# Performance work log

Hardware: AMD Instinct MI355X
Metric: run time of the kernel (lower is better)

Reference implementation:

```python
import jax, jax.numpy as jnp
import numpy as np

SEQ, NSTEPS = 8192, 2048
IDIM, HDIM, NL = 256, 1024, 4


def setup_inputs() -> dict:
    key = jax.random.key(0)
    ks = jax.random.split(key, 6)
    s = 0.02  # small init so tanh recurrence stays well-conditioned
    return {
        "xs": jax.random.normal(ks[0], (SEQ, IDIM), dtype=jnp.float32),
        "Wx0": jax.random.normal(ks[1], (IDIM, HDIM), dtype=jnp.float32) * s,
        "Wh0": jax.random.normal(ks[2], (HDIM, HDIM), dtype=jnp.float32) * s,
        "b0": jnp.zeros((HDIM,), dtype=jnp.float32),
        "Wx_rest": jax.random.normal(ks[3], (NL - 1, HDIM, HDIM), dtype=jnp.float32) * s,
        "Wh_rest": jax.random.normal(ks[4], (NL - 1, HDIM, HDIM), dtype=jnp.float32) * s,
        "b_rest": jnp.zeros((NL - 1, HDIM), dtype=jnp.float32),
        "out_W": jax.random.normal(ks[5], (IDIM, HDIM), dtype=jnp.float32) * s,  # eqx Linear: (out, in)
        "out_b": jnp.zeros((IDIM,), dtype=jnp.float32),
        "n_steps": NSTEPS,
    }


def _layer_scan(xs, Wx, Wh, b):
    # open-loop scan of one tanh RNN cell over the whole sequence
    pre = xs @ Wx + b  # (T, H): hoist input projection out of the scan

    def step(h, p):
        h = jnp.tanh(p + h @ Wh)
        return h, h

    h0 = jnp.zeros((Wh.shape[0],), dtype=xs.dtype)
    last, outs = jax.lax.scan(step, h0, pre)
    return last, outs


def reference(xs, Wx0, Wh0, b0, Wx_rest, Wh_rest, b_rest, out_W, out_b, n_steps):
    # open_loop: run each layer's scan over the full sequence
    states = []
    h, seq = _layer_scan(xs, Wx0, Wh0, b0)
    states.append(h)
    for i in range(Wx_rest.shape[0]):
        h, seq = _layer_scan(seq, Wx_rest[i], Wh_rest[i], b_rest[i])
        states.append(h)
    ol_outs = seq @ out_W.T + out_b  # (T, IDIM) vmap'd out_layer

    def ar_step(carry, _):
        sts, x = carry
        new_sts = []
        h = jnp.tanh(x @ Wx0 + sts[0] @ Wh0 + b0)
        new_sts.append(h)
        x = h
        for i in range(Wx_rest.shape[0]):
            h = jnp.tanh(x @ Wx_rest[i] + sts[i + 1] @ Wh_rest[i] + b_rest[i])
            new_sts.append(h)
            x = h
        x = out_W @ x + out_b
        return (tuple(new_sts), x), x

    carry = (tuple(states), ol_outs[-1])
    _, ar_outs = jax.lax.scan(ar_step, carry, None, length=n_steps)
    return jnp.concatenate([ol_outs, ar_outs], axis=0)  # (T + n_steps, IDIM)
```

## Files before the change

kernel.cpp:

```cpp
#include <hip/hip_runtime.h>
#include <math.h>

#define SEQ    8192
#define NSTEPS 2048
#define NTOT   (SEQ + NSTEPS)
#define IDIM   256
#define HDIM   1024

#define NWG    256
#define TPB    256
#define WPB    4
#define RD     8

typedef unsigned long long u64;

#define WT_FLOATS   (8ull*HDIM*HDIM)
#define BF_FLOAT    WT_FLOATS
#define RING_FLOAT  (WT_FLOATS + HDIM)
#define RING_U64S   (4ull*RD*HDIM)
#define PROG_FLOAT  (RING_FLOAT + 2ull*RING_U64S)


__global__ void k_fuse_w(const float* __restrict__ outW, const float* __restrict__ Wx0,
                         float* __restrict__ ws) {
    int l = blockIdx.x * 256 + threadIdx.x;
    int j = blockIdx.y;
    float acc = 0.f;
    for (int k = 0; k < IDIM; ++k)
        acc += outW[(size_t)k * HDIM + l] * Wx0[(size_t)k * HDIM + j];
    ws[(size_t)j * HDIM + l] = acc;
}

__global__ void k_fuse_b(const float* __restrict__ b0, const float* __restrict__ outb,
                         const float* __restrict__ Wx0, float* __restrict__ ws) {
    int j = blockIdx.x * 256 + threadIdx.x;
    float acc = b0[j];
    for (int k = 0; k < IDIM; ++k)
        acc += outb[k] * Wx0[(size_t)k * HDIM + j];
    ws[BF_FLOAT + j] = acc;
}

__global__ void k_pack(const float* __restrict__ Wh0, const float* __restrict__ Wxr,
                       const float* __restrict__ Whr, float* __restrict__ ws) {
    __shared__ float t[32][33];
    int z = blockIdx.z;
    const float* src; int slot;
    if (z == 0)      { src = Wh0;                                  slot = 1; }
    else if (z <= 3) { src = Wxr + (size_t)(z - 1) * HDIM * HDIM;  slot = 2 * z; }
    else             { src = Whr + (size_t)(z - 4) * HDIM * HDIM;  slot = 2 * (z - 4) + 3; }
    int j0 = blockIdx.x * 32, l0 = blockIdx.y * 32;
    t[threadIdx.y][threadIdx.x] = src[(size_t)(l0 + threadIdx.y) * HDIM + j0 + threadIdx.x];
    __syncthreads();
    float* dst = ws + (size_t)slot * HDIM * HDIM;
    dst[(size_t)(j0 + threadIdx.y) * HDIM + (l0 + threadIdx.x)] = t[threadIdx.x][threadIdx.y];
}

__global__ void k_init(float* __restrict__ ws) {
    int t = blockIdx.x * blockDim.x + threadIdx.x;
    ((u64*)(ws + RING_FLOAT))[t] = 0ull;
    if (t < NWG) ((unsigned*)(ws + PROG_FLOAT))[t] = 0u;
}


__device__ __forceinline__ float wsum(float v) {
#pragma unroll
    for (int off = 32; off > 0; off >>= 1) v += __shfl_xor(v, off, 64);
    return v;
}

__device__ __forceinline__ void capture_vec(const u64* slot, unsigned want,
                                            float* dst, int lane) {
    for (;;) {
        u64 v[16]; bool ok = true;
#pragma unroll
        for (int k = 0; k < 16; ++k) {
            v[k] = __hip_atomic_load(slot + lane + 64 * k, __ATOMIC_RELAXED, __HIP_MEMORY_SCOPE_AGENT);
            ok &= ((unsigned)(v[k] >> 32) == want);
        }
        if (__all(ok)) {
#pragma unroll
            for (int k = 0; k < 16; ++k) dst[lane + 64 * k] = __uint_as_float((unsigned)v[k]);
            return;
        }
    }
}

__global__ __launch_bounds__(TPB, 1) void k_scan(
    const float* __restrict__ xs, const float* __restrict__ Wx0,
    const float* __restrict__ b0, const float* __restrict__ brest,
    const float* __restrict__ outW, const float* __restrict__ outb,
    float* __restrict__ ws, float* __restrict__ out)
{
    const int lane  = threadIdx.x & 63;
    const int wv    = threadIdx.x >> 6;
    const int layer = blockIdx.x >> 6;
    const int wgl   = blockIdx.x & 63;
    const int jw    = wgl * WPB + wv;
    const int j0    = jw * 4;

    __shared__ float ldsOwn[2][HDIM];
    __shared__ float ldsUp[2][HDIM];

    u64* ring = (u64*)(ws + RING_FLOAT);
    unsigned* prog = (unsigned*)(ws + PROG_FLOAT);
    const int cons = (layer + 1) & 3;

    float A[4][16], B[4][16];
#pragma unroll
    for (int c = 0; c < 4; ++c)
#pragma unroll
        for (int k = 0; k < 16; ++k) {
            A[c][k] = ws[((size_t)(2 * layer) * HDIM + (j0 + c)) * HDIM + lane + 64 * k];
            B[c][k] = ws[((size_t)(2 * layer + 1) * HDIM + (j0 + c)) * HDIM + lane + 64 * k];
        }
    float wx0[4][4];
    if (layer == 0) {
#pragma unroll
        for (int c = 0; c < 4; ++c)
#pragma unroll
            for (int k = 0; k < 4; ++k)
                wx0[c][k] = Wx0[(size_t)(lane + 64 * k) * HDIM + (j0 + c)];
    }
    float ow[16]; float obv = 0.f;
    if (layer == 3) {
#pragma unroll
        for (int k = 0; k < 16; ++k) ow[k] = outW[(size_t)jw * HDIM + lane + 64 * k];
        obv = outb[jw];
    }
    float bb[4], bfc[4];
#pragma unroll
    for (int c = 0; c < 4; ++c) {
        bb[c]  = (layer == 0) ? b0[j0 + c] : brest[(size_t)(layer - 1) * HDIM + j0 + c];
        bfc[c] = (layer == 0) ? ws[BF_FLOAT + j0 + c] : 0.f;
    }

    int minp = 0;

    for (int n = 1; n <= NTOT; ++n) {
        const int par = n & 1;
        const bool xphase = (layer == 0) && (n <= SEQ);

        float xv[4];
        if (xphase) {
            const float* xr = xs + (size_t)(n - 1) * IDIM;
#pragma unroll
            for (int k = 0; k < 4; ++k) xv[k] = xr[lane + 64 * k];
        }

        if (wv == 0) {
            capture_vec(ring + ((size_t)layer * RD + ((n - 1) & (RD - 1))) * HDIM,
                        (unsigned)(n - 1), ldsOwn[par], lane);
        } else if (wv == 1 && !xphase) {
            const int ul = (layer == 0) ? 3 : layer - 1;
            const unsigned want = (layer == 0) ? (unsigned)(n - 1) : (unsigned)n;
            capture_vec(ring + ((size_t)ul * RD + (want & (RD - 1))) * HDIM,
                        want, ldsUp[par], lane);
        }
        __syncthreads();
        if (wv == 0 && lane == 0)
            __hip_atomic_store(&prog[blockIdx.x], (unsigned)n, __ATOMIC_RELAXED, __HIP_MEMORY_SCOPE_AGENT);

        float a0 = 0.f, a1 = 0.f, a2 = 0.f, a3 = 0.f;
        if (xphase) {
#pragma unroll
            for (int k = 0; k < 4; ++k) {
                float x = xv[k];
                a0 += x * wx0[0][k]; a1 += x * wx0[1][k]; a2 += x * wx0[2][k]; a3 += x * wx0[3][k];
            }
        } else {
#pragma unroll
            for (int k = 0; k < 16; ++k) {
                float x = ldsUp[par][lane + 64 * k];
                a0 += x * A[0][k]; a1 += x * A[1][k]; a2 += x * A[2][k]; a3 += x * A[3][k];
            }
        }
#pragma unroll
        for (int k = 0; k < 16; ++k) {
            float y = ldsOwn[par][lane + 64 * k];
            a0 += y * B[0][k]; a1 += y * B[1][k]; a2 += y * B[2][k]; a3 += y * B[3][k];
        }
        a0 = wsum(a0); a1 = wsum(a1); a2 = wsum(a2); a3 = wsum(a3);
        const bool fph = (layer == 0) && (n > SEQ);
        float r0 = tanhf(a0 + (fph ? bfc[0] : bb[0]));
        float r1 = tanhf(a1 + (fph ? bfc[1] : bb[1]));
        float r2 = tanhf(a2 + (fph ? bfc[2] : bb[2]));
        float r3 = tanhf(a3 + (fph ? bfc[3] : bb[3]));

        if (minp < (int)n - 7) {
            for (;;) {
                unsigned pv = __hip_atomic_load(&prog[cons * 64 + lane],
                                                __ATOMIC_RELAXED, __HIP_MEMORY_SCOPE_AGENT);
#pragma unroll
                for (int off = 32; off > 0; off >>= 1) {
                    unsigned o = (unsigned)__shfl_xor((int)pv, off, 64);
                    pv = pv < o ? pv : o;
                }
                minp = (int)pv;
                if (minp >= (int)n - 7) break;
                __builtin_amdgcn_s_sleep(2);
            }
        }

        {
            u64* dst = ring + ((size_t)layer * RD + (n & (RD - 1))) * HDIM + j0;
            if (lane < 4) {
                float v = (lane == 0) ? r0 : (lane == 1) ? r1 : (lane == 2) ? r2 : r3;
                __hip_atomic_store(dst + lane,
                                   ((u64)(unsigned)n << 32) | (u64)__float_as_uint(v),
                                   __ATOMIC_RELAXED, __HIP_MEMORY_SCOPE_AGENT);
            }
        }

        if (layer == 3 && n >= 2) {
            float a = 0.f;
#pragma unroll
            for (int k = 0; k < 16; ++k) a += ldsOwn[par][lane + 64 * k] * ow[k];
            a = wsum(a);
            if (lane == 0) out[(size_t)(n - 2) * IDIM + jw] = a + obv;
        }
    }

    if (layer == 3) {
        if (wv == 0)
            capture_vec(ring + ((size_t)3 * RD + (NTOT & (RD - 1))) * HDIM,
                        (unsigned)NTOT, ldsOwn[0], lane);
        __syncthreads();
        float a = 0.f;
#pragma unroll
        for (int k = 0; k < 16; ++k) a += ldsOwn[0][lane + 64 * k] * ow[k];
        a = wsum(a);
        if (lane == 0) out[(size_t)(NTOT - 1) * IDIM + jw] = a + obv;
    }
}


extern "C" void kernel_launch(void* const* d_in, const int* in_sizes, int n_in,
                              void* d_out, int out_size, void* d_ws, size_t ws_size,
                              hipStream_t stream) {
    (void)in_sizes; (void)n_in; (void)out_size; (void)ws_size;
    const float* xs   = (const float*)d_in[0];
    const float* Wx0  = (const float*)d_in[1];
    const float* Wh0  = (const float*)d_in[2];
    const float* b0   = (const float*)d_in[3];
    const float* Wxr  = (const float*)d_in[4];
    const float* Whr  = (const float*)d_in[5];
    const float* brst = (const float*)d_in[6];
    const float* outW = (const float*)d_in[7];
    const float* outb = (const float*)d_in[8];
    float* ws  = (float*)d_ws;
    float* out = (float*)d_out;

    k_fuse_w<<<dim3(4, HDIM), dim3(256), 0, stream>>>(outW, Wx0, ws);
    k_fuse_b<<<dim3(4), dim3(256), 0, stream>>>(b0, outb, Wx0, ws);
    k_pack<<<dim3(32, 32, 7), dim3(32, 32), 0, stream>>>(Wh0, Wxr, Whr, ws);
    k_init<<<dim3(64), dim3(512), 0, stream>>>(ws);

    void* args[] = { (void*)&xs, (void*)&Wx0, (void*)&b0, (void*)&brst,
                     (void*)&outW, (void*)&outb, (void*)&ws, (void*)&out };
    hipError_t e = hipLaunchCooperativeKernel((void*)k_scan, dim3(NWG), dim3(TPB),
                                              args, 0, stream);
    if (e != hipSuccess) {
        k_scan<<<dim3(NWG), dim3(TPB), 0, stream>>>(xs, Wx0, b0, brst, outW, outb, ws, out);
    }
}
```

Before: 51.43 ms.

## Halve workgroups, split ring capture across waves, move backpressure wait, fast tanh

```diff
diff --git a/kernel.cpp b/kernel.cpp
--- a/kernel.cpp
+++ b/kernel.cpp
@@ -7,9 +7,9 @@
 #define IDIM   256
 #define HDIM   1024
 
-#define NWG    256
-#define TPB    256
-#define WPB    4
+#define NWG    128
+#define TPB    512
+#define WPB    8
 #define RD     8
 
 typedef unsigned long long u64;
@@ -68,20 +68,32 @@
     return v;
 }
 
-__device__ __forceinline__ void capture_vec(const u64* slot, unsigned want,
-                                            float* dst, int lane) {
+__device__ __forceinline__ float ftanh(float x) {
+    x = fminf(15.f, fmaxf(-15.f, x));
+    float e = __builtin_amdgcn_exp2f(x * 2.8853900817779268f);
+    return (e - 1.f) * __builtin_amdgcn_rcpf(e + 1.f);
+}
+
+__device__ __forceinline__ void capture8(const u64* slot, unsigned want,
+                                         float* dst, int lane, int kbase) {
+    unsigned done = 0;
     for (;;) {
-        u64 v[16]; bool ok = true;
-#pragma unroll
-        for (int k = 0; k < 16; ++k) {
-            v[k] = __hip_atomic_load(slot + lane + 64 * k, __ATOMIC_RELAXED, __HIP_MEMORY_SCOPE_AGENT);
-            ok &= ((unsigned)(v[k] >> 32) == want);
-        }
-        if (__all(ok)) {
-#pragma unroll
-            for (int k = 0; k < 16; ++k) dst[lane + 64 * k] = __uint_as_float((unsigned)v[k]);
-            return;
-        }
+        u64 v[8];
+#pragma unroll
+        for (int k = 0; k < 8; ++k) {
+            v[k] = 0;
+            if (!(done & (1u << k)))
+                v[k] = __hip_atomic_load(slot + lane + 64 * (kbase + k),
+                                         __ATOMIC_RELAXED, __HIP_MEMORY_SCOPE_AGENT);
+        }
+#pragma unroll
+        for (int k = 0; k < 8; ++k) {
+            if (!(done & (1u << k)) && ((unsigned)(v[k] >> 32) == want)) {
+                dst[lane + 64 * (kbase + k)] = __uint_as_float((unsigned)v[k]);
+                done |= 1u << k;
+            }
+        }
+        if (__all(done == 0xFFu)) return;
     }
 }
 
@@ -93,8 +105,8 @@
 {
     const int lane  = threadIdx.x & 63;
     const int wv    = threadIdx.x >> 6;
-    const int layer = blockIdx.x >> 6;
-    const int wgl   = blockIdx.x & 63;
+    const int layer = blockIdx.x >> 5;
+    const int wgl   = blockIdx.x & 31;
     const int jw    = wgl * WPB + wv;
     const int j0    = jw * 4;
 
@@ -140,55 +152,9 @@
         const int par = n & 1;
         const bool xphase = (layer == 0) && (n <= SEQ);
 
-        float xv[4];
-        if (xphase) {
-            const float* xr = xs + (size_t)(n - 1) * IDIM;
-#pragma unroll
-            for (int k = 0; k < 4; ++k) xv[k] = xr[lane + 64 * k];
-        }
-
-        if (wv == 0) {
-            capture_vec(ring + ((size_t)layer * RD + ((n - 1) & (RD - 1))) * HDIM,
-                        (unsigned)(n - 1), ldsOwn[par], lane);
-        } else if (wv == 1 && !xphase) {
-            const int ul = (layer == 0) ? 3 : layer - 1;
-            const unsigned want = (layer == 0) ? (unsigned)(n - 1) : (unsigned)n;
-            capture_vec(ring + ((size_t)ul * RD + (want & (RD - 1))) * HDIM,
-                        want, ldsUp[par], lane);
-        }
-        __syncthreads();
-        if (wv == 0 && lane == 0)
-            __hip_atomic_store(&prog[blockIdx.x], (unsigned)n, __ATOMIC_RELAXED, __HIP_MEMORY_SCOPE_AGENT);
-
-        float a0 = 0.f, a1 = 0.f, a2 = 0.f, a3 = 0.f;
-        if (xphase) {
-#pragma unroll
-            for (int k = 0; k < 4; ++k) {
-                float x = xv[k];
-                a0 += x * wx0[0][k]; a1 += x * wx0[1][k]; a2 += x * wx0[2][k]; a3 += x * wx0[3][k];
-            }
-        } else {
-#pragma unroll
-            for (int k = 0; k < 16; ++k) {
-                float x = ldsUp[par][lane + 64 * k];
-                a0 += x * A[0][k]; a1 += x * A[1][k]; a2 += x * A[2][k]; a3 += x * A[3][k];
-            }
-        }
-#pragma unroll
-        for (int k = 0; k < 16; ++k) {
-            float y = ldsOwn[par][lane + 64 * k];
-            a0 += y * B[0][k]; a1 += y * B[1][k]; a2 += y * B[2][k]; a3 += y * B[3][k];
-        }
-        a0 = wsum(a0); a1 = wsum(a1); a2 = wsum(a2); a3 = wsum(a3);
-        const bool fph = (layer == 0) && (n > SEQ);
-        float r0 = tanhf(a0 + (fph ? bfc[0] : bb[0]));
-        float r1 = tanhf(a1 + (fph ? bfc[1] : bb[1]));
-        float r2 = tanhf(a2 + (fph ? bfc[2] : bb[2]));
-        float r3 = tanhf(a3 + (fph ? bfc[3] : bb[3]));
-
-        if (minp < (int)n - 7) {
+        if (minp < n - 7) {
             for (;;) {
-                unsigned pv = __hip_atomic_load(&prog[cons * 64 + lane],
+                unsigned pv = __hip_atomic_load(&prog[cons * 32 + (lane & 31)],
                                                 __ATOMIC_RELAXED, __HIP_MEMORY_SCOPE_AGENT);
 #pragma unroll
                 for (int off = 32; off > 0; off >>= 1) {
@@ -196,10 +162,56 @@
                     pv = pv < o ? pv : o;
                 }
                 minp = (int)pv;
-                if (minp >= (int)n - 7) break;
+                if (minp >= n - 7) break;
                 __builtin_amdgcn_s_sleep(2);
             }
         }
+
+        float xv[4];
+        if (xphase) {
+            const float* xr = xs + (size_t)(n - 1) * IDIM;
+#pragma unroll
+            for (int k = 0; k < 4; ++k) xv[k] = xr[lane + 64 * k];
+        }
+
+        if (wv < 2) {
+            capture8(ring + ((size_t)layer * RD + ((n - 1) & (RD - 1))) * HDIM,
+                     (unsigned)(n - 1), ldsOwn[par], lane, wv * 8);
+        } else if (wv < 4 && !xphase) {
+            const int ul = (layer == 0) ? 3 : layer - 1;
+            const unsigned want = (layer == 0) ? (unsigned)(n - 1) : (unsigned)n;
+            capture8(ring + ((size_t)ul * RD + (want & (RD - 1))) * HDIM,
+                     want, ldsUp[par], lane, (wv - 2) * 8);
+        }
+        __syncthreads();
+        if (threadIdx.x == 0)
+            __hip_atomic_store(&prog[blockIdx.x], (unsigned)n, __ATOMIC_RELAXED, __HIP_MEMORY_SCOPE_AGENT);
+
+        float a0 = 0.f, a1 = 0.f, a2 = 0.f, a3 = 0.f;
+        if (xphase) {
+#pragma unroll
+            for (int k = 0; k < 4; ++k) {
+                float x = xv[k];
+                a0 += x * wx0[0][k]; a1 += x * wx0[1][k]; a2 += x * wx0[2][k]; a3 += x * wx0[3][k];
+            }
+        } else {
+#pragma unroll
+            for (int k = 0; k < 16; ++k) {
+                float x = ldsUp[par][lane + 64 * k];
+                a0 += x * A[0][k]; a1 += x * A[1][k]; a2 += x * A[2][k]; a3 += x * A[3][k];
+            }
+        }
+#pragma unroll
+        for (int k = 0; k < 16; ++k) {
+            float y = ldsOwn[par][lane + 64 * k];
+            a0 += y * B[0][k]; a1 += y * B[1][k]; a2 += y * B[2][k]; a3 += y * B[3][k];
+        }
+        a0 = wsum(a0); a1 = wsum(a1); a2 = wsum(a2); a3 = wsum(a3);
+        const bool fph = (layer == 0) && (n > SEQ);
+        float r0 = ftanh(a0 + (fph ? bfc[0] : bb[0]));
+        float r1 = ftanh(a1 + (fph ? bfc[1] : bb[1]));
+        float r2 = ftanh(a2 + (fph ? bfc[2] : bb[2]));
+        float r3 = ftanh(a3 + (fph ? bfc[3] : bb[3]));
 
         {
             u64* dst = ring + ((size_t)layer * RD + (n & (RD - 1))) * HDIM + j0;
@@ -221,9 +233,9 @@
     }
 
     if (layer == 3) {
-        if (wv == 0)
-            capture_vec(ring + ((size_t)3 * RD + (NTOT & (RD - 1))) * HDIM,
-                        (unsigned)NTOT, ldsOwn[0], lane);
+        if (wv < 2)
+            capture8(ring + ((size_t)3 * RD + (NTOT & (RD - 1))) * HDIM,
+                     (unsigned)NTOT, ldsOwn[0], lane, wv * 8);
         __syncthreads();
         float a = 0.f;
 #pragma unroll
```

Result: faster. 50.00 ms (-2.8%).
